# Optimization experiments

Measured on AMD Instinct MI355X. Metric: run time of the kernel, lower is better.

## Reference

```python
import jax, jax.numpy as jnp
import numpy as np

B, N, D = 32, 64, 256
PENALTY = 10000.0
TEMP = 0.05
N_ITERS = 20


def setup_inputs() -> dict:
    key = jax.random.key(0)
    ks = jax.random.split(key, 8)
    f32 = jnp.float32
    return {
        "slots_t": jax.random.normal(ks[0], (B, N, D), f32),
        "slots_t1": jax.random.normal(ks[1], (B, N, D), f32),
        "alive_t": jax.random.uniform(ks[2], (B, N), f32),
        "alive_t1": jax.random.uniform(ks[3], (B, N), f32),
        "W1": jax.random.normal(ks[4], (3 * D, D), f32) / np.float32(np.sqrt(3 * D)),
        "b1": jnp.zeros((D,), f32),
        "W2": jax.random.normal(ks[5], (D, D // 4), f32) / np.float32(np.sqrt(D)),
        "b2": jnp.zeros((D // 4,), f32),
        "W3": jax.random.normal(ks[6], (D // 4, 1), f32) / np.float32(np.sqrt(D // 4)),
        "b3": jnp.zeros((1,), f32),
    }


def reference(slots_t, slots_t1, alive_t, alive_t1, W1, b1, W2, b2, W3, b3):
    # ---- cost matrix: pairwise expand + tiny MLP ----
    s_t = jnp.clip(slots_t, -50.0, 50.0)    # (B,N,D)
    s_t1 = jnp.clip(slots_t1, -50.0, 50.0)  # (B,N,D)
    s_t_exp = jnp.broadcast_to(s_t[:, :, None, :], (B, N, N, D))
    s_t1_exp = jnp.broadcast_to(s_t1[:, None, :, :], (B, N, N, D))
    diff = jnp.abs(s_t_exp - s_t1_exp)
    pair_feat = jnp.concatenate([s_t_exp, s_t1_exp, diff], axis=-1)  # (B,N,N,3D)
    h = jax.nn.relu(pair_feat @ W1 + b1)       # (B,N,N,D)
    h = jax.nn.relu(h @ W2 + b2)               # (B,N,N,D/4)
    score = (h @ W3 + b3)[..., 0]              # (B,N,N)
    dead_t = (alive_t < 0.5).astype(score.dtype)
    dead_t1 = (alive_t1 < 0.5).astype(score.dtype)
    score = score - PENALTY * dead_t[:, :, None] - PENALTY * dead_t1[:, None, :]
    cost = jnp.clip(-score, -PENALTY, PENALTY)
    # ---- Sinkhorn (log-space) ----
    log_alpha = -cost / TEMP

    def step(la, _):
        la = la - jax.nn.logsumexp(la, axis=2, keepdims=True)
        la = la - jax.nn.logsumexp(la, axis=1, keepdims=True)
        return la, None

    log_alpha, _ = jax.lax.scan(step, log_alpha, None, length=N_ITERS)
    assignment = jnp.exp(log_alpha)            # (B,N,N)
    perm = jnp.argmax(assignment, axis=2)      # (B,N)
    confidence = jnp.max(assignment, axis=2)   # (B,N)
    # ---- matched mask ----
    alive_t_hard = (alive_t > 0.5).astype(assignment.dtype)
    alive_t1_hard = (alive_t1 > 0.5).astype(assignment.dtype)
    matched_t1 = jnp.take_along_axis(alive_t1_hard, perm, axis=1)
    matched = alive_t_hard * matched_t1 * (confidence > 0.3).astype(assignment.dtype)
    return perm, matched
```

## Files before the change

### kernel.cpp

```cpp
#include <hip/hip_runtime.h>

#define NB 32
#define NN 64
#define ND 256
#define MH 32
constexpr float PEN = 10000.0f;
constexpr float TEMP_ = 0.05f;

typedef __bf16 bfrag __attribute__((ext_vector_type(8)));
typedef float  f32x4 __attribute__((ext_vector_type(4)));

__device__ __forceinline__ float clip50(float x) { return fminf(fmaxf(x, -50.0f), 50.0f); }

__device__ __forceinline__ ushort bf16_rne(float x) {
    uint u = __builtin_bit_cast(uint, x);
    return (ushort)((u + 0x7fffu + ((u >> 16) & 1u)) >> 16);
}
__device__ __forceinline__ void split2(float a, float b, uint& h, uint& l) {
    const ushort ha = bf16_rne(a), hb = bf16_rne(b);
    const float fa = __builtin_bit_cast(float, (uint)ha << 16);
    const float fb = __builtin_bit_cast(float, (uint)hb << 16);
    const ushort la = bf16_rne(a - fa), lb = bf16_rne(b - fb);
    h = (uint)ha | ((uint)hb << 16);
    l = (uint)la | ((uint)lb << 16);
}
#define ASW(m, k2) ((m) * 512 + ((k2) ^ (((m) & 7) << 4)))

__global__ __launch_bounds__(256)
void k01_uv_pack(const float* __restrict__ s_t, const float* __restrict__ s_t1,
                 const float* __restrict__ W1, const float* __restrict__ b1,
                 const float* __restrict__ W2, float* __restrict__ U,
                 float* __restrict__ V, ushort* __restrict__ w1h,
                 ushort* __restrict__ w1l, ushort* __restrict__ w2h,
                 ushort* __restrict__ w2l)
{
    const int tid = threadIdx.x;
    if (blockIdx.x >= 512) {
        const int gid = (blockIdx.x - 512) * 256 + tid;
        const float* srcW; ushort *dh, *dl;
        int fb, kt, col, kbase, stride, base;
        if (gid < 8192) {
            fb = gid >> 6; kt = fb >> 4;
            const int ntg = fb & 15, ln = gid & 63;
            col = ntg * 16 + (ln & 15); kbase = kt * 32 + (ln >> 4) * 8;
            srcW = W1 + 2 * ND * ND; stride = ND; dh = w1h; dl = w1l; base = gid * 8;
        } else {
            const int g2 = gid - 8192;
            fb = g2 >> 6; kt = fb >> 2;
            const int ntg = fb & 3, ln = g2 & 63;
            col = ntg * 16 + (ln & 15); kbase = kt * 32 + (ln >> 4) * 8;
            srcW = W2; stride = 64; dh = w2h; dl = w2l; base = g2 * 8;
        }
        uint hv[4], lv[4];
        #pragma unroll
        for (int p = 0; p < 4; ++p) {
            const float a = srcW[(kbase + 2 * p) * stride + col];
            const float b = srcW[(kbase + 2 * p + 1) * stride + col];
            split2(a, b, hv[p], lv[p]);
        }
        *(uint4*)(dh + base) = make_uint4(hv[0], hv[1], hv[2], hv[3]);
        *(uint4*)(dl + base) = make_uint4(lv[0], lv[1], lv[2], lv[3]);
        return;
    }
    const int half = blockIdx.x >> 8;
    const int rem  = blockIdx.x & 255;
    const int rb   = rem >> 1;
    const int colh = rem & 1;
    const float* src = half ? s_t1 : s_t;
    const float* W   = W1 + half * ND * ND;
    float* dst = half ? V : U;
    __shared__ float sL[16 * ND];
    const int rbase = rb * 16;
    #pragma unroll
    for (int t = 0; t < 4; ++t) {
        const int i4 = ((t << 8) + tid) << 2;
        float4 a = *(const float4*)(src + rbase * ND + i4);
        a.x = clip50(a.x); a.y = clip50(a.y); a.z = clip50(a.z); a.w = clip50(a.w);
        *(float4*)(sL + i4) = a;
    }
    __syncthreads();
    const int wv   = tid >> 6;
    const int lane = tid & 63;
    const int tj1  = lane >> 5;
    const int tc   = lane & 31;
    const int r0   = wv * 4 + tj1 * 2;
    const int c0   = colh * 128 + tc * 4;
    float acc[2][4] = {};
    for (int k4 = 0; k4 < ND; k4 += 4) {
        float4 sv[2];
        #pragma unroll
        for (int r = 0; r < 2; ++r) sv[r] = *(const float4*)(sL + (r0 + r) * ND + k4);
        #pragma unroll
        for (int kk = 0; kk < 4; ++kk) {
            const float4 wvv = *(const float4*)(W + (k4 + kk) * ND + c0);
            #pragma unroll
            for (int r = 0; r < 2; ++r) {
                const float s = (&sv[r].x)[kk];
                acc[r][0] = fmaf(s, wvv.x, acc[r][0]);
                acc[r][1] = fmaf(s, wvv.y, acc[r][1]);
                acc[r][2] = fmaf(s, wvv.z, acc[r][2]);
                acc[r][3] = fmaf(s, wvv.w, acc[r][3]);
            }
        }
    }
    float4 bias = make_float4(0.f, 0.f, 0.f, 0.f);
    if (!half) bias = *(const float4*)(b1 + c0);
    #pragma unroll
    for (int r = 0; r < 2; ++r) {
        float4 o;
        o.x = acc[r][0] + bias.x; o.y = acc[r][1] + bias.y;
        o.z = acc[r][2] + bias.z; o.w = acc[r][3] + bias.w;
        *(float4*)(dst + (rbase + r0 + r) * ND + c0) = o;
    }
}

__global__ __launch_bounds__(256, 4)
void k2_scores(const float* __restrict__ s_t, const float* __restrict__ s_t1,
               const float* __restrict__ b2, const float* __restrict__ W3,
               const float* __restrict__ b3, const float* __restrict__ alive_t,
               const float* __restrict__ alive_t1,
               const float* __restrict__ U, const float* __restrict__ V,
               const ushort* __restrict__ w1h, const ushort* __restrict__ w1l,
               const ushort* __restrict__ w2h, const ushort* __restrict__ w2l,
               float* __restrict__ laG)
{
    __shared__ ushort sAh[MH * ND];
    __shared__ ushort sAl[MH * ND];
    __shared__ float  red[4 * MH];
    const int tid = threadIdx.x;
    const int bi  = blockIdx.x >> 1;
    const int jh  = blockIdx.x & 1;
    const int b   = bi >> 6;
    const int jbase = jh * MH;
    const int lane = tid & 63;
    const int w    = tid >> 6;
    const int mlane = lane & 15;
    const int kg    = lane >> 4;

    {
        const float* stb = s_t + bi * ND;
        const float* s1b = s_t1 + (size_t)b * NN * ND + (size_t)jbase * ND;
        #pragma unroll
        for (int t = 0; t < 4; ++t) {
            const int slot = (t << 8) + tid;
            const int m  = slot >> 5;
            const int k0 = (slot & 31) << 3;
            const float4 a0 = *(const float4*)(stb + k0);
            const float4 a1 = *(const float4*)(stb + k0 + 4);
            const float4 p0 = *(const float4*)(s1b + m * ND + k0);
            const float4 p1 = *(const float4*)(s1b + m * ND + k0 + 4);
            float d[8];
            d[0] = fabsf(clip50(a0.x) - clip50(p0.x));
            d[1] = fabsf(clip50(a0.y) - clip50(p0.y));
            d[2] = fabsf(clip50(a0.z) - clip50(p0.z));
            d[3] = fabsf(clip50(a0.w) - clip50(p0.w));
            d[4] = fabsf(clip50(a1.x) - clip50(p1.x));
            d[5] = fabsf(clip50(a1.y) - clip50(p1.y));
            d[6] = fabsf(clip50(a1.z) - clip50(p1.z));
            d[7] = fabsf(clip50(a1.w) - clip50(p1.w));
            uint hv[4], lv[4];
            #pragma unroll
            for (int p = 0; p < 4; ++p) split2(d[2*p], d[2*p+1], hv[p], lv[p]);
            const int off = ASW(m, k0 * 2);
            *(uint4*)((char*)sAh + off) = make_uint4(hv[0], hv[1], hv[2], hv[3]);
            *(uint4*)((char*)sAl + off) = make_uint4(lv[0], lv[1], lv[2], lv[3]);
        }
    }
    __syncthreads();

    f32x4 acc[2][4];
    #pragma unroll
    for (int mt = 0; mt < 2; ++mt)
        #pragma unroll
        for (int nt = 0; nt < 4; ++nt)
            #pragma unroll
            for (int r = 0; r < 4; ++r) acc[mt][nt][r] = 0.f;
    #pragma unroll
    for (int kt = 0; kt < 8; ++kt) {
        bfrag Bh[4], Bl[4], Ah[2], Al[2];
        #pragma unroll
        for (int nt = 0; nt < 4; ++nt) {
            const int fo = (kt * 16 + (w << 2) + nt) * 512 + lane * 8;
            Bh[nt] = *(const bfrag*)(w1h + fo);
            Bl[nt] = *(const bfrag*)(w1l + fo);
        }
        const int k2b = (kt * 32 + kg * 8) * 2;
        #pragma unroll
        for (int mt = 0; mt < 2; ++mt) {
            const int m = mt * 16 + mlane;
            const int off = ASW(m, k2b);
            Ah[mt] = *(const bfrag*)((const char*)sAh + off);
            Al[mt] = *(const bfrag*)((const char*)sAl + off);
        }
        #pragma unroll
        for (int mt = 0; mt < 2; ++mt)
            #pragma unroll
            for (int nt = 0; nt < 4; ++nt) {
                acc[mt][nt] = __builtin_amdgcn_mfma_f32_16x16x32_bf16(Ah[mt], Bh[nt], acc[mt][nt], 0, 0, 0);
                acc[mt][nt] = __builtin_amdgcn_mfma_f32_16x16x32_bf16(Ah[mt], Bl[nt], acc[mt][nt], 0, 0, 0);
                acc[mt][nt] = __builtin_amdgcn_mfma_f32_16x16x32_bf16(Al[mt], Bh[nt], acc[mt][nt], 0, 0, 0);
            }
    }
    __syncthreads();

    {
        const float* Ur = U + (size_t)bi * ND;
        const float* Vb = V + (size_t)b * NN * ND + (size_t)jbase * ND;
        float Uc[4];
        #pragma unroll
        for (int nt = 0; nt < 4; ++nt) Uc[nt] = Ur[w * 64 + nt * 16 + mlane];
        #pragma unroll
        for (int mt = 0; mt < 2; ++mt) {
            #pragma unroll
            for (int r = 0; r < 4; ++r) {
                const int j = mt * 16 + (kg << 2) + r;
                const float* Vr = Vb + (size_t)j * ND;
                #pragma unroll
                for (int nt = 0; nt < 4; ++nt) {
                    const int c = w * 64 + nt * 16 + mlane;
                    float x = acc[mt][nt][r] + Uc[nt] + Vr[c];
                    x = fmaxf(x, 0.f);
                    const ushort hh = bf16_rne(x);
                    const float  fh = __builtin_bit_cast(float, (uint)hh << 16);
                    const ushort ll = bf16_rne(x - fh);
                    const int off = ASW(j, c * 2);
                    *(ushort*)((char*)sAh + off) = hh;
                    *(ushort*)((char*)sAl + off) = ll;
                }
            }
        }
    }
    __syncthreads();

    f32x4 acc2[2];
    #pragma unroll
    for (int mt = 0; mt < 2; ++mt)
        #pragma unroll
        for (int r = 0; r < 4; ++r) acc2[mt][r] = 0.f;
    #pragma unroll
    for (int kt = 0; kt < 8; ++kt) {
        const int fo = (kt * 4 + w) * 512 + lane * 8;
        const bfrag Bh = *(const bfrag*)(w2h + fo);
        const bfrag Bl = *(const bfrag*)(w2l + fo);
        const int k2b = (kt * 32 + kg * 8) * 2;
        #pragma unroll
        for (int mt = 0; mt < 2; ++mt) {
            const int m = mt * 16 + mlane;
            const int off = ASW(m, k2b);
            const bfrag Ah = *(const bfrag*)((const char*)sAh + off);
            const bfrag Al = *(const bfrag*)((const char*)sAl + off);
            acc2[mt] = __builtin_amdgcn_mfma_f32_16x16x32_bf16(Ah, Bh, acc2[mt], 0, 0, 0);
            acc2[mt] = __builtin_amdgcn_mfma_f32_16x16x32_bf16(Ah, Bl, acc2[mt], 0, 0, 0);
            acc2[mt] = __builtin_amdgcn_mfma_f32_16x16x32_bf16(Al, Bh, acc2[mt], 0, 0, 0);
        }
    }

    {
        const int m = w * 16 + mlane;
        const float b2v = b2[m];
        const float w3v = W3[m];
        #pragma unroll
        for (int mt = 0; mt < 2; ++mt) {
            #pragma unroll
            for (int r = 0; r < 4; ++r) {
                const int j = mt * 16 + (kg << 2) + r;
                float val = fmaxf(acc2[mt][r] + b2v, 0.f) * w3v;
                val += __shfl_xor(val, 1, 64);
                val += __shfl_xor(val, 2, 64);
                val += __shfl_xor(val, 4, 64);
                val += __shfl_xor(val, 8, 64);
                if (mlane == 0) red[w * MH + j] = val;
            }
        }
    }
    __syncthreads();
    if (tid < MH) {
        const int j = tid;
        const float sc = red[j] + red[MH + j] + red[2 * MH + j] + red[3 * MH + j] + b3[0];
        const float pen_i = (alive_t[bi] < 0.5f) ? PEN : 0.0f;
        const float pj = (alive_t1[b * NN + jbase + j] < 0.5f) ? PEN : 0.0f;
        const float sp = sc - pen_i - pj;
        laG[bi * NN + jbase + j] = fminf(fmaxf(sp, -PEN), PEN) / TEMP_;
    }
}

__global__ __launch_bounds__(256)
void k3_sinkhorn(const float* __restrict__ laG, const float* __restrict__ alive_t,
                 const float* __restrict__ alive_t1, float* __restrict__ out)
{
    __shared__ float la[NN * 65];
    const int b = blockIdx.x, tid = threadIdx.x;
    for (int idx = tid; idx < NN * NN; idx += 256)
        la[(idx >> 6) * 65 + (idx & 63)] = laG[b * NN * NN + idx];
    __syncthreads();

    const int g = tid >> 2;
    const int q = tid & 3;
    for (int it = 0; it < 20; ++it) {
        {
            float m = -INFINITY;
            #pragma unroll
            for (int t = 0; t < 16; ++t) m = fmaxf(m, la[g * 65 + q * 16 + t]);
            m = fmaxf(m, __shfl_xor(m, 1, 64));
            m = fmaxf(m, __shfl_xor(m, 2, 64));
            float s = 0.f;
            #pragma unroll
            for (int t = 0; t < 16; ++t) s += expf(la[g * 65 + q * 16 + t] - m);
            s += __shfl_xor(s, 1, 64);
            s += __shfl_xor(s, 2, 64);
            const float lse = m + logf(s);
            #pragma unroll
            for (int t = 0; t < 16; ++t) la[g * 65 + q * 16 + t] -= lse;
        }
        __syncthreads();
        {
            float m = -INFINITY;
            #pragma unroll
            for (int t = 0; t < 16; ++t) m = fmaxf(m, la[(q * 16 + t) * 65 + g]);
            m = fmaxf(m, __shfl_xor(m, 1, 64));
            m = fmaxf(m, __shfl_xor(m, 2, 64));
            float s = 0.f;
            #pragma unroll
            for (int t = 0; t < 16; ++t) s += expf(la[(q * 16 + t) * 65 + g] - m);
            s += __shfl_xor(s, 1, 64);
            s += __shfl_xor(s, 2, 64);
            const float lse = m + logf(s);
            #pragma unroll
            for (int t = 0; t < 16; ++t) la[(q * 16 + t) * 65 + g] -= lse;
        }
        __syncthreads();
    }

    float bm = -INFINITY; int bidx = 0;
    #pragma unroll
    for (int t = 0; t < 16; ++t) {
        const float v = la[g * 65 + q * 16 + t];
        if (v > bm) { bm = v; bidx = q * 16 + t; }
    }
    #pragma unroll
    for (int off = 1; off < 4; off <<= 1) {
        const float om = __shfl_xor(bm, off, 64);
        const int   oi = __shfl_xor(bidx, off, 64);
        if (om > bm || (om == bm && oi < bidx)) { bm = om; bidx = oi; }
    }
    if (q == 0) {
        const float conf = expf(bm);
        const float at  = alive_t[b * NN + g];
        const float at1 = alive_t1[b * NN + bidx];
        const float matched = (at > 0.5f && at1 > 0.5f && conf > 0.3f) ? 1.0f : 0.0f;
        out[b * NN + g] = (float)bidx;
        out[NB * NN + b * NN + g] = matched;
    }
}

extern "C" void kernel_launch(void* const* d_in, const int* in_sizes, int n_in,
                              void* d_out, int out_size, void* d_ws, size_t ws_size,
                              hipStream_t stream)
{
    (void)in_sizes; (void)n_in; (void)out_size; (void)ws_size;
    const float* s_t      = (const float*)d_in[0];
    const float* s_t1     = (const float*)d_in[1];
    const float* alive_t  = (const float*)d_in[2];
    const float* alive_t1 = (const float*)d_in[3];
    const float* W1 = (const float*)d_in[4];
    const float* b1 = (const float*)d_in[5];
    const float* W2 = (const float*)d_in[6];
    const float* b2 = (const float*)d_in[7];
    const float* W3 = (const float*)d_in[8];
    const float* b3 = (const float*)d_in[9];

    char* ws = (char*)d_ws;
    float*  U   = (float*)(ws);
    float*  V   = (float*)(ws + 2097152);
    float*  laG = (float*)(ws + 4194304);
    ushort* w1h = (ushort*)(ws + 4718592);
    ushort* w1l = (ushort*)(ws + 4849664);
    ushort* w2h = (ushort*)(ws + 4980736);
    ushort* w2l = (ushort*)(ws + 5013504);
    float* out = (float*)d_out;

    hipLaunchKernelGGL(k01_uv_pack, dim3(552), dim3(256), 0, stream,
                       s_t, s_t1, W1, b1, W2, U, V, w1h, w1l, w2h, w2l);
    hipLaunchKernelGGL(k2_scores, dim3(NB * NN * 2), dim3(256), 0, stream,
                       s_t, s_t1, b2, W3, b3, alive_t, alive_t1, U, V,
                       w1h, w1l, w2h, w2l, laG);
    hipLaunchKernelGGL(k3_sinkhorn, dim3(NB), dim3(256), 0, stream,
                       laG, alive_t, alive_t1, out);
}
```

Baseline: 207.7 us.

## Pipeline diff-feature staging with MFMA k-steps and widen Sinkhorn blocks

In the score kernel, the absolute-difference feature tile is now built in four K-chunks of 64. The load of the next chunk is issued while the MFMA steps for the previous chunk run, so global-load latency can overlap with matrix math instead of the whole tile being staged before any MFMA starts. This costs extra barriers and more live registers. Separately, the Sinkhorn kernel goes from 256 to 512 threads, with 8 lanes per row or column, to halve the serial work per thread in each logsumexp.

```diff
diff --git a/kernel.cpp b/kernel.cpp
--- a/kernel.cpp
+++ b/kernel.cpp
@@ -11,7 +11,6 @@
 typedef float  f32x4 __attribute__((ext_vector_type(4)));
 
 __device__ __forceinline__ float clip50(float x) { return fminf(fmaxf(x, -50.0f), 50.0f); }
-
 __device__ __forceinline__ ushort bf16_rne(float x) {
     uint u = __builtin_bit_cast(uint, x);
     return (ushort)((u + 0x7fffu + ((u >> 16) & 1u)) >> 16);
@@ -137,36 +136,32 @@
     const int mlane = lane & 15;
     const int kg    = lane >> 4;
 
-    {
-        const float* stb = s_t + bi * ND;
-        const float* s1b = s_t1 + (size_t)b * NN * ND + (size_t)jbase * ND;
-        #pragma unroll
-        for (int t = 0; t < 4; ++t) {
-            const int slot = (t << 8) + tid;
-            const int m  = slot >> 5;
-            const int k0 = (slot & 31) << 3;
-            const float4 a0 = *(const float4*)(stb + k0);
-            const float4 a1 = *(const float4*)(stb + k0 + 4);
-            const float4 p0 = *(const float4*)(s1b + m * ND + k0);
-            const float4 p1 = *(const float4*)(s1b + m * ND + k0 + 4);
-            float d[8];
-            d[0] = fabsf(clip50(a0.x) - clip50(p0.x));
-            d[1] = fabsf(clip50(a0.y) - clip50(p0.y));
-            d[2] = fabsf(clip50(a0.z) - clip50(p0.z));
-            d[3] = fabsf(clip50(a0.w) - clip50(p0.w));
-            d[4] = fabsf(clip50(a1.x) - clip50(p1.x));
-            d[5] = fabsf(clip50(a1.y) - clip50(p1.y));
-            d[6] = fabsf(clip50(a1.z) - clip50(p1.z));
-            d[7] = fabsf(clip50(a1.w) - clip50(p1.w));
-            uint hv[4], lv[4];
-            #pragma unroll
-            for (int p = 0; p < 4; ++p) split2(d[2*p], d[2*p+1], hv[p], lv[p]);
-            const int off = ASW(m, k0 * 2);
-            *(uint4*)((char*)sAh + off) = make_uint4(hv[0], hv[1], hv[2], hv[3]);
-            *(uint4*)((char*)sAl + off) = make_uint4(lv[0], lv[1], lv[2], lv[3]);
-        }
-    }
-    __syncthreads();
+    const float* stb = s_t + bi * ND;
+    const float* s1b = s_t1 + (size_t)b * NN * ND + (size_t)jbase * ND;
+    const int m1  = tid >> 3;
+    const int kk1 = (tid & 7) << 3;
+
+    float4 cA0, cA1, cP0, cP1;
+
+#define P1LOAD(T) do { const int k0_ = (T) * 64 + kk1; \
+    cA0 = *(const float4*)(stb + k0_);      cA1 = *(const float4*)(stb + k0_ + 4); \
+    cP0 = *(const float4*)(s1b + m1 * ND + k0_); cP1 = *(const float4*)(s1b + m1 * ND + k0_ + 4); } while (0)
+
+#define P1STORE(T) do { \
+    const float d0 = fabsf(clip50(cA0.x) - clip50(cP0.x)); \
+    const float d1 = fabsf(clip50(cA0.y) - clip50(cP0.y)); \
+    const float d2 = fabsf(clip50(cA0.z) - clip50(cP0.z)); \
+    const float d3 = fabsf(clip50(cA0.w) - clip50(cP0.w)); \
+    const float d4 = fabsf(clip50(cA1.x) - clip50(cP1.x)); \
+    const float d5 = fabsf(clip50(cA1.y) - clip50(cP1.y)); \
+    const float d6 = fabsf(clip50(cA1.z) - clip50(cP1.z)); \
+    const float d7 = fabsf(clip50(cA1.w) - clip50(cP1.w)); \
+    uint hv0, hv1, hv2, hv3, lv0, lv1, lv2, lv3; \
+    split2(d0, d1, hv0, lv0); split2(d2, d3, hv1, lv1); \
+    split2(d4, d5, hv2, lv2); split2(d6, d7, hv3, lv3); \
+    const int off_ = ASW(m1, ((T) * 64 + kk1) * 2); \
+    *(uint4*)((char*)sAh + off_) = make_uint4(hv0, hv1, hv2, hv3); \
+    *(uint4*)((char*)sAl + off_) = make_uint4(lv0, lv1, lv2, lv3); } while (0)
 
     f32x4 acc[2][4];
     #pragma unroll
@@ -175,32 +170,40 @@
         for (int nt = 0; nt < 4; ++nt)
             #pragma unroll
             for (int r = 0; r < 4; ++r) acc[mt][nt][r] = 0.f;
-    #pragma unroll
-    for (int kt = 0; kt < 8; ++kt) {
-        bfrag Bh[4], Bl[4], Ah[2], Al[2];
-        #pragma unroll
-        for (int nt = 0; nt < 4; ++nt) {
-            const int fo = (kt * 16 + (w << 2) + nt) * 512 + lane * 8;
-            Bh[nt] = *(const bfrag*)(w1h + fo);
-            Bl[nt] = *(const bfrag*)(w1l + fo);
-        }
-        const int k2b = (kt * 32 + kg * 8) * 2;
-        #pragma unroll
-        for (int mt = 0; mt < 2; ++mt) {
-            const int m = mt * 16 + mlane;
-            const int off = ASW(m, k2b);
-            Ah[mt] = *(const bfrag*)((const char*)sAh + off);
-            Al[mt] = *(const bfrag*)((const char*)sAl + off);
-        }
-        #pragma unroll
-        for (int mt = 0; mt < 2; ++mt)
-            #pragma unroll
-            for (int nt = 0; nt < 4; ++nt) {
-                acc[mt][nt] = __builtin_amdgcn_mfma_f32_16x16x32_bf16(Ah[mt], Bh[nt], acc[mt][nt], 0, 0, 0);
-                acc[mt][nt] = __builtin_amdgcn_mfma_f32_16x16x32_bf16(Ah[mt], Bl[nt], acc[mt][nt], 0, 0, 0);
-                acc[mt][nt] = __builtin_amdgcn_mfma_f32_16x16x32_bf16(Al[mt], Bh[nt], acc[mt][nt], 0, 0, 0);
-            }
-    }
+
+#define P2KT(KT) do { \
+    bfrag Bh_[4], Bl_[4], Ah_[2], Al_[2]; \
+    _Pragma("unroll") for (int nt = 0; nt < 4; ++nt) { \
+        const int fo_ = ((KT) * 16 + (w << 2) + nt) * 512 + lane * 8; \
+        Bh_[nt] = *(const bfrag*)(w1h + fo_); \
+        Bl_[nt] = *(const bfrag*)(w1l + fo_); } \
+    const int k2b_ = ((KT) * 32 + kg * 8) * 2; \
+    _Pragma("unroll") for (int mt = 0; mt < 2; ++mt) { \
+        const int off_ = ASW(mt * 16 + mlane, k2b_); \
+        Ah_[mt] = *(const bfrag*)((const char*)sAh + off_); \
+        Al_[mt] = *(const bfrag*)((const char*)sAl + off_); } \
+    _Pragma("unroll") for (int mt = 0; mt < 2; ++mt) \
+    _Pragma("unroll") for (int nt = 0; nt < 4; ++nt) { \
+        acc[mt][nt] = __builtin_amdgcn_mfma_f32_16x16x32_bf16(Ah_[mt], Bh_[nt], acc[mt][nt], 0, 0, 0); \
+        acc[mt][nt] = __builtin_amdgcn_mfma_f32_16x16x32_bf16(Ah_[mt], Bl_[nt], acc[mt][nt], 0, 0, 0); \
+        acc[mt][nt] = __builtin_amdgcn_mfma_f32_16x16x32_bf16(Al_[mt], Bh_[nt], acc[mt][nt], 0, 0, 0); } \
+    } while (0)
+
+    P1LOAD(0); P1STORE(0);
+    P1LOAD(1);
+    __syncthreads();
+    P2KT(0); P2KT(1);
+    P1STORE(1);
+    P1LOAD(2);
+    __syncthreads();
+    P2KT(2); P2KT(3);
+    P1STORE(2);
+    P1LOAD(3);
+    __syncthreads();
+    P2KT(4); P2KT(5);
+    P1STORE(3);
+    __syncthreads();
+    P2KT(6); P2KT(7);
     __syncthreads();
 
     {
@@ -284,61 +287,65 @@
     }
 }
 
-__global__ __launch_bounds__(256)
+__global__ __launch_bounds__(512)
 void k3_sinkhorn(const float* __restrict__ laG, const float* __restrict__ alive_t,
                  const float* __restrict__ alive_t1, float* __restrict__ out)
 {
     __shared__ float la[NN * 65];
     const int b = blockIdx.x, tid = threadIdx.x;
-    for (int idx = tid; idx < NN * NN; idx += 256)
+    for (int idx = tid; idx < NN * NN; idx += 512)
         la[(idx >> 6) * 65 + (idx & 63)] = laG[b * NN * NN + idx];
     __syncthreads();
 
-    const int g = tid >> 2;
-    const int q = tid & 3;
+    const int g = tid >> 3;
+    const int q = tid & 7;
     for (int it = 0; it < 20; ++it) {
         {
             float m = -INFINITY;
             #pragma unroll
-            for (int t = 0; t < 16; ++t) m = fmaxf(m, la[g * 65 + q * 16 + t]);
+            for (int t = 0; t < 8; ++t) m = fmaxf(m, la[g * 65 + q * 8 + t]);
             m = fmaxf(m, __shfl_xor(m, 1, 64));
             m = fmaxf(m, __shfl_xor(m, 2, 64));
+            m = fmaxf(m, __shfl_xor(m, 4, 64));
             float s = 0.f;
             #pragma unroll
-            for (int t = 0; t < 16; ++t) s += expf(la[g * 65 + q * 16 + t] - m);
+            for (int t = 0; t < 8; ++t) s += expf(la[g * 65 + q * 8 + t] - m);
             s += __shfl_xor(s, 1, 64);
             s += __shfl_xor(s, 2, 64);
+            s += __shfl_xor(s, 4, 64);
             const float lse = m + logf(s);
             #pragma unroll
-            for (int t = 0; t < 16; ++t) la[g * 65 + q * 16 + t] -= lse;
+            for (int t = 0; t < 8; ++t) la[g * 65 + q * 8 + t] -= lse;
         }
         __syncthreads();
         {
             float m = -INFINITY;
             #pragma unroll
-            for (int t = 0; t < 16; ++t) m = fmaxf(m, la[(q * 16 + t) * 65 + g]);
+            for (int t = 0; t < 8; ++t) m = fmaxf(m, la[(q * 8 + t) * 65 + g]);
             m = fmaxf(m, __shfl_xor(m, 1, 64));
             m = fmaxf(m, __shfl_xor(m, 2, 64));
+            m = fmaxf(m, __shfl_xor(m, 4, 64));
             float s = 0.f;
             #pragma unroll
-            for (int t = 0; t < 16; ++t) s += expf(la[(q * 16 + t) * 65 + g] - m);
+            for (int t = 0; t < 8; ++t) s += expf(la[(q * 8 + t) * 65 + g] - m);
             s += __shfl_xor(s, 1, 64);
             s += __shfl_xor(s, 2, 64);
+            s += __shfl_xor(s, 4, 64);
             const float lse = m + logf(s);
             #pragma unroll
-            for (int t = 0; t < 16; ++t) la[(q * 16 + t) * 65 + g] -= lse;
+            for (int t = 0; t < 8; ++t) la[(q * 8 + t) * 65 + g] -= lse;
         }
         __syncthreads();
     }
 
     float bm = -INFINITY; int bidx = 0;
     #pragma unroll
-    for (int t = 0; t < 16; ++t) {
-        const float v = la[g * 65 + q * 16 + t];
-        if (v > bm) { bm = v; bidx = q * 16 + t; }
-    }
-    #pragma unroll
-    for (int off = 1; off < 4; off <<= 1) {
+    for (int t = 0; t < 8; ++t) {
+        const float v = la[g * 65 + q * 8 + t];
+        if (v > bm) { bm = v; bidx = q * 8 + t; }
+    }
+    #pragma unroll
+    for (int off = 1; off < 8; off <<= 1) {
         const float om = __shfl_xor(bm, off, 64);
         const int   oi = __shfl_xor(bidx, off, 64);
         if (om > bm || (om == bm && oi < bidx)) { bm = om; bidx = oi; }
@@ -384,6 +391,6 @@
     hipLaunchKernelGGL(k2_scores, dim3(NB * NN * 2), dim3(256), 0, stream,
                        s_t, s_t1, b2, W3, b3, alive_t, alive_t1, U, V,
                        w1h, w1l, w2h, w2l, laG);
-    hipLaunchKernelGGL(k3_sinkhorn, dim3(NB), dim3(256), 0, stream,
+    hipLaunchKernelGGL(k3_sinkhorn, dim3(NB), dim3(512), 0, stream,
                        laG, alive_t, alive_t1, out);
 }
```

New measurement: 205.2 us. About the same (-1.2%).
